# Kernel optimization log

Hardware: AMD Instinct MI355X
Metric: run time of the kernel (lower is better)

## Reference

```python
import math
import jax, jax.numpy as jnp
import numpy as np

B, L, D = 2, 2048, 512
H, DK, RANK, NH = 8, 64, 32, 1
K_MAX = 64
BANDWIDTH = 8.0
N_BUCKETS = 16


def setup_inputs() -> dict:
    key = jax.random.key(0)
    ks = jax.random.split(key, 14)
    s = 0.02
    return {
        "query": jax.random.normal(ks[0], (B, L, D), jnp.float32),
        "key": jax.random.normal(ks[1], (B, L, D), jnp.float32),
        "value": jax.random.normal(ks[2], (B, L, D), jnp.float32),
        "Wq": jax.random.normal(ks[3], (D, H * DK), jnp.float32) * s,
        "bq": jnp.zeros((H * DK,), jnp.float32),
        "Wk": jax.random.normal(ks[4], (D, H * DK), jnp.float32) * s,
        "bk": jnp.zeros((H * DK,), jnp.float32),
        "Wv": jax.random.normal(ks[5], (D, H * DK), jnp.float32) * s,
        "bv": jnp.zeros((H * DK,), jnp.float32),
        "U": jax.random.normal(ks[6], (H, DK, RANK), jnp.float32) * s,
        "V": jax.random.normal(ks[7], (H, RANK, D), jnp.float32) * s,
        "rv": jax.random.normal(ks[8], (H, DK, NH), jnp.float32),  # LSH random vectors (buffer)
        "Wo": jax.random.normal(ks[9], (H * D, D), jnp.float32) * s,
        "bo": jnp.zeros((D,), jnp.float32),
    }


def _lsh_hash(x, r):
    # binary quantize then bucketed floor hash: [B,L,dk] @ [dk,nh] -> [B,L,nh]
    xb = (x > 0).astype(x.dtype)
    return jnp.floor((xb @ r) / BANDWIDTH) % N_BUCKETS


def reference(query, key, value, Wq, bq, Wk, bk, Wv, bv, U, V, rv, Wo, bo):
    Bq, Lq, Dm = query.shape
    nheads, dk = U.shape[0], U.shape[1]
    q = (query @ Wq + bq).reshape(Bq, Lq, nheads, dk).transpose(0, 2, 1, 3)  # [B,H,L,dk]
    k = (key @ Wk + bk).reshape(Bq, Lq, nheads, dk).transpose(0, 2, 1, 3)
    v = (value @ Wv + bv).reshape(Bq, Lq, nheads, dk).transpose(0, 2, 1, 3)
    scale = math.sqrt(dk)  # optimized_sqrt(d_key), d_key power of two

    head_outputs = []
    for h in range(nheads):
        qh, kh, vh = q[:, h], k[:, h], v[:, h]  # [B,L,dk]
        qhash = _lsh_hash(qh, rv[h])  # [B,L,nh]
        khash = _lsh_hash(kh, rv[h])
        # [B,L,L] candidate match matrix (all hashes equal)
        matches = (qhash[:, :, None, :] == khash[:, None, :, :]).all(-1)
        # first K_MAX matching key indices in ascending order (== torch nonzero order)
        order = jnp.argsort(jnp.logical_not(matches), axis=-1, stable=True)
        cand = order[:, :, :K_MAX]  # [B,L,k_max]
        valid = jnp.take_along_axis(matches, cand, axis=-1)  # [B,L,k_max]
        ckeys = jnp.take_along_axis(kh[:, None, :, :], cand[..., None], axis=2)  # [B,L,k_max,dk]
        cvals = jnp.take_along_axis(vh[:, None, :, :], cand[..., None], axis=2)
        sim = jnp.einsum('bld,blkd->blk', qh, ckeys) / scale
        sim = jnp.where(valid, sim, -jnp.inf)
        attn = jax.nn.softmax(sim, axis=-1)  # invalid slots get exactly 0 weight
        # attention-weighted sum then low-rank up-projection (linear, so commutes
        # with the weighted sum; avoids the [B,L,k_max,d_model] intermediate)
        ctx = jnp.einsum('blk,blkd->bld', attn, cvals)  # [B,L,dk]
        head_outputs.append((ctx @ U[h]) @ V[h])  # [B,L,d_model]

    concat = jnp.concatenate(head_outputs, axis=-1)  # [B,L,H*d_model]
    return concat @ Wo + bo
```

## Files before the change

kernel.cpp:

```cpp
#include <hip/hip_runtime.h>
#include <math.h>

#define Bb 2
#define Ll 2048
#define Dd 512
#define Hh 8
#define DKq 64
#define NBUCK 16
#define KMAX 64
#define MAX_ITEMS 2304

__device__ __forceinline__ void gl_lds16(const float* g, float* l) {
  __builtin_amdgcn_global_load_lds(
      (const __attribute__((address_space(1))) void*)g,
      (__attribute__((address_space(3))) void*)l, 16, 0, 0);
}

#define VM_WAIT(N)                                                \
  do {                                                            \
    asm volatile("s_waitcnt vmcnt(" #N ")" ::: "memory");         \
    __builtin_amdgcn_sched_barrier(0);                            \
  } while (0)

__global__ __launch_bounds__(64) void proj_kernel(
    const float* __restrict__ Xq, const float* __restrict__ Xk, const float* __restrict__ Xv,
    const float* __restrict__ Wq, const float* __restrict__ Wk, const float* __restrict__ Wv,
    const float* __restrict__ bq, const float* __restrict__ bk, const float* __restrict__ bv,
    float* __restrict__ qb, float* __restrict__ kb, float* __restrict__ vb)
{
  const float *X, *W, *bias; float* dst;
  if (blockIdx.z == 0)      { X=Xq; W=Wq; bias=bq; dst=qb; }
  else if (blockIdx.z == 1) { X=Xk; W=Wk; bias=bk; dst=kb; }
  else                      { X=Xv; W=Wv; bias=bv; dst=vb; }
  __shared__ float Bs[3][16 * 64];
  const int lane = threadIdx.x;
  const int m0 = blockIdx.y * 32;
  const int n0 = blockIdx.x * 64;
  const int tx = lane & 15, ty = lane >> 4;

  const float* bSrc[4];
  #pragma unroll
  for (int j = 0; j < 4; j++) {
    int krow = 4*j + (lane >> 4);
    bSrc[j] = W + (size_t)krow * 512 + n0 + ((lane & 15) << 2);
  }
  const float* Arow[8];
  #pragma unroll
  for (int i = 0; i < 8; i++) Arow[i] = X + (size_t)(m0 + ty*8 + i) * 512;

  #pragma unroll
  for (int j = 0; j < 4; j++) gl_lds16(bSrc[j],                  &Bs[0][j*256]);
  #pragma unroll
  for (int j = 0; j < 4; j++) gl_lds16(bSrc[j] + (size_t)16*512, &Bs[1][j*256]);

  float acc[8][4] = {};
  int rd = 0, wr = 2;
  for (int t = 0; t < 32; t++) {
    if (t < 30) {
      const int ks = (t + 2) * 16;
      #pragma unroll
      for (int j = 0; j < 4; j++) gl_lds16(bSrc[j] + (size_t)ks*512, &Bs[wr][j*256]);
    }
    if (t == 0)       VM_WAIT(8);
    else if (t < 30)  VM_WAIT(40);
    else if (t == 30) VM_WAIT(36);
    else              VM_WAIT(32);

    const float* Bc = &Bs[rd][0];
    const int k0 = t * 16;
    float4 a[8], an[8];
    #pragma unroll
    for (int i = 0; i < 8; i++) a[i] = *(const float4*)&Arow[i][k0];
    #pragma unroll
    for (int kk4 = 0; kk4 < 4; kk4++) {
      if (kk4 < 3) {
        #pragma unroll
        for (int i = 0; i < 8; i++)
          an[i] = *(const float4*)&Arow[i][k0 + (kk4 + 1) * 4];
      }
      #pragma unroll
      for (int s = 0; s < 4; s++) {
        const int kk = kk4*4 + s;
        float4 b0 = *(const float4*)&Bc[kk*64 + tx*4];
        #pragma unroll
        for (int i = 0; i < 8; i++) {
          const float as = (s==0) ? a[i].x : (s==1) ? a[i].y
                         : (s==2) ? a[i].z : a[i].w;
          acc[i][0] += as * b0.x;  acc[i][1] += as * b0.y;
          acc[i][2] += as * b0.z;  acc[i][3] += as * b0.w;
        }
      }
      if (kk4 < 3) {
        #pragma unroll
        for (int i = 0; i < 8; i++) a[i] = an[i];
      }
    }
    rd = (rd == 2) ? 0 : rd + 1;
    wr = (wr == 2) ? 0 : wr + 1;
  }

  const int head = n0 >> 6;
  const int d0 = tx * 4;
  #pragma unroll
  for (int i = 0; i < 8; i++) {
    int m = m0 + ty*8 + i;
    int b = m >> 11, l = m & 2047;
    float* drow = &dst[(((size_t)b*Hh + head)*Ll + l)*DKq];
    #pragma unroll
    for (int j = 0; j < 4; j++) drow[d0 + j] = acc[i][j] + bias[n0 + tx*4 + j];
  }
}

__global__ __launch_bounds__(256) void hash_kernel(
    const float* __restrict__ qb, const float* __restrict__ kb,
    const float* __restrict__ rv, int* __restrict__ qhash, int* __restrict__ khash)
{
  int gwave = (blockIdx.x * blockDim.x + threadIdx.x) >> 6;
  int lane = threadIdx.x & 63;
  const int NR = Bb * Hh * Ll;
  if (gwave >= 2 * NR) return;
  int isK = gwave >= NR;
  int row = isK ? gwave - NR : gwave;
  int h = (row >> 11) & 7;
  const float* src = isK ? kb : qb;
  float x = src[(size_t)row * DKq + lane];
  float r = rv[h * DKq + lane];
  float v = (x > 0.0f) ? r : 0.0f;
  #pragma unroll
  for (int off = 32; off; off >>= 1) v += __shfl_xor(v, off);
  if (lane == 0) {
    float fb = floorf(v * 0.125f);
    int ib = (int)fb;
    int bucket = ib & 15;
    (isK ? khash : qhash)[row] = bucket;
  }
}

__global__ __launch_bounds__(256) void bucket_kernel(
    const int* __restrict__ qhash, const int* __restrict__ khash,
    int* __restrict__ qlist, int* __restrict__ kcand,
    int4* __restrict__ items, int* __restrict__ nitems)
{
  const int bh = blockIdx.x;
  const int tid = threadIdx.x;
  __shared__ int cnt[NBUCK], cur[NBUCK], off[NBUCK + 1], kc[NBUCK];
  if (tid < NBUCK) cnt[tid] = 0;
  __syncthreads();
  const int* qh = &qhash[bh * Ll];
  for (int l = tid; l < Ll; l += 256) atomicAdd(&cnt[qh[l]], 1);
  __syncthreads();
  if (tid == 0) {
    int s = 0;
    for (int i = 0; i < NBUCK; i++) { off[i] = s; cur[i] = s; s += cnt[i]; }
    off[NBUCK] = s;
  }
  __syncthreads();
  for (int l = tid; l < Ll; l += 256) {
    int p = atomicAdd(&cur[qh[l]], 1);
    qlist[bh * Ll + p] = l;
  }
  const int lane = tid & 63, w = tid >> 6;
  const int* kh = &khash[bh * Ll];
  for (int bi = 0; bi < 4; bi++) {
    int bucket = w * 4 + bi;
    int* cl = &kcand[((size_t)bh * NBUCK + bucket) * KMAX];
    int total = 0;
    for (int c0 = 0; c0 < Ll && total < KMAX; c0 += 64) {
      int hv = kh[c0 + lane];
      unsigned long long mm = __ballot(hv == bucket);
      int pre = __popcll(mm & ((1ULL << lane) - 1ULL));
      if (hv == bucket && total + pre < KMAX) cl[total + pre] = c0 + lane;
      total += __popcll(mm);
    }
    if (lane == 0) kc[bucket] = total < KMAX ? total : KMAX;
  }
  __syncthreads();
  if (tid < NBUCK) {
    const int bucket = tid;
    int nq = off[bucket + 1] - off[bucket];
    int cb = kc[bucket];
    int n = (cb > 0) ? ((nq + 15) >> 4) : 0;
    if (n > 0) {
      int base = atomicAdd(nitems, n);
      for (int i = 0; i < n; i++) {
        int q0 = 16 * i;
        int qn = nq - q0; if (qn > 16) qn = 16;
        items[base + i] = make_int4(bh * NBUCK + bucket, off[bucket] + q0, qn, cb);
      }
    }
  }
}

__device__ __forceinline__ void lds_fence() {
  asm volatile("s_waitcnt lgkmcnt(0)" ::: "memory");
  __builtin_amdgcn_sched_barrier(0);
}

__global__ __launch_bounds__(256, 2) void attn_kernel(
    const float* __restrict__ qb, const float* __restrict__ kb, const float* __restrict__ vb,
    const int* __restrict__ qlist, const int* __restrict__ kcand,
    const int4* __restrict__ items, const int* __restrict__ nitems,
    float* __restrict__ ctx)
{
  __shared__ float qs_all[4][16 * 64];
  __shared__ float sa_all[4][128];
  const int wid = threadIdx.x >> 6, lane = threadIdx.x & 63;
  const int idx = blockIdx.x * 4 + wid;
  if (idx >= nitems[0]) return;
  const int4 it = items[idx];
  const int code = it.x, qstart = it.y, qn = it.z, cnt = it.w;
  const int bh = code >> 4;
  float* qs = qs_all[wid];
  float* sa = sa_all[wid];

  const float* qbh = qb + (size_t)bh * Ll * DKq;
  const float* kbh = kb + (size_t)bh * Ll * DKq;
  const float* vbh = vb + (size_t)bh * Ll * DKq;

  int qidx_v = (lane < qn)  ? qlist[bh * Ll + qstart + lane] : 0;
  int cidx_v = (lane < cnt) ? kcand[(size_t)code * KMAX + lane] : 0;

  float4 kr[16];
  {
    const float4* krow = (const float4*)kbh + (size_t)cidx_v * 16;
    #pragma unroll
    for (int i = 0; i < 16; i++) kr[i] = krow[i];
  }
  float vt[64];
  #pragma unroll
  for (int c = 0; c < 64; c++) {
    int rowc = __shfl(cidx_v, c);
    vt[c] = vbh[(size_t)rowc * DKq + lane];
  }
  #pragma unroll
  for (int i = 0; i < 4; i++) {
    int f = lane + 64 * i;
    int r = f >> 4, c4 = f & 15;
    int qrow = __shfl(qidx_v, r);
    float4 qv = *((const float4*)qbh + (size_t)qrow * 16 + c4);
    *(float4*)&qs[r * 64 + c4 * 4] = qv;
  }
  lds_fence();

  const int b = bh >> 3, h = bh & 7;
  const float4* qs4 = (const float4*)qs;
  const float4* sa4 = (const float4*)sa;

  for (int jj = 0; jj < qn; jj += 2) {
    const int j0  = jj;
    const int j1v = jj + 1;
    const int j1r = (j1v < qn) ? j1v : j0;
    float p00=0.f,p01=0.f,p02=0.f,p03=0.f;
    float p10=0.f,p11=0.f,p12=0.f,p13=0.f;
    #pragma unroll
    for (int i = 0; i < 16; i += 4) {
      float4 qA0 = qs4[j0*16 + i + 0];
      float4 qA1 = qs4[j0*16 + i + 1];
      float4 qA2 = qs4[j0*16 + i + 2];
      float4 qA3 = qs4[j0*16 + i + 3];
      float4 qB0 = qs4[j1r*16 + i + 0];
      float4 qB1 = qs4[j1r*16 + i + 1];
      float4 qB2 = qs4[j1r*16 + i + 2];
      float4 qB3 = qs4[j1r*16 + i + 3];
      p00 += qA0.x*kr[i+0].x + qA0.y*kr[i+0].y + qA0.z*kr[i+0].z + qA0.w*kr[i+0].w;
      p01 += qA1.x*kr[i+1].x + qA1.y*kr[i+1].y + qA1.z*kr[i+1].z + qA1.w*kr[i+1].w;
      p02 += qA2.x*kr[i+2].x + qA2.y*kr[i+2].y + qA2.z*kr[i+2].z + qA2.w*kr[i+2].w;
      p03 += qA3.x*kr[i+3].x + qA3.y*kr[i+3].y + qA3.z*kr[i+3].z + qA3.w*kr[i+3].w;
      p10 += qB0.x*kr[i+0].x + qB0.y*kr[i+0].y + qB0.z*kr[i+0].z + qB0.w*kr[i+0].w;
      p11 += qB1.x*kr[i+1].x + qB1.y*kr[i+1].y + qB1.z*kr[i+1].z + qB1.w*kr[i+1].w;
      p12 += qB2.x*kr[i+2].x + qB2.y*kr[i+2].y + qB2.z*kr[i+2].z + qB2.w*kr[i+2].w;
      p13 += qB3.x*kr[i+3].x + qB3.y*kr[i+3].y + qB3.z*kr[i+3].z + qB3.w*kr[i+3].w;
    }
    float sA = ((p00 + p01) + (p02 + p03)) * 0.125f;
    float sB = ((p10 + p11) + (p12 + p13)) * 0.125f;
    sA = (lane < cnt) ? sA : -INFINITY;
    sB = (lane < cnt) ? sB : -INFINITY;
    float mA = sA, mB = sB;
    #pragma unroll
    for (int off = 32; off; off >>= 1) {
      mA = fmaxf(mA, __shfl_xor(mA, off));
      mB = fmaxf(mB, __shfl_xor(mB, off));
    }
    float eA = __expf(sA - mA);
    float eB = __expf(sB - mB);
    float sumA = eA, sumB = eB;
    #pragma unroll
    for (int off = 32; off; off >>= 1) {
      sumA += __shfl_xor(sumA, off);
      sumB += __shfl_xor(sumB, off);
    }
    lds_fence();
    sa[lane]      = eA;
    sa[64 + lane] = eB;
    lds_fence();
    float c00=0.f,c01=0.f,c02=0.f,c03=0.f;
    float c10=0.f,c11=0.f,c12=0.f,c13=0.f;
    #pragma unroll
    for (int i = 0; i < 16; i++) {
      float4 aA = sa4[i];
      float4 aB = sa4[16 + i];
      c00 += aA.x * vt[4*i + 0];
      c01 += aA.y * vt[4*i + 1];
      c02 += aA.z * vt[4*i + 2];
      c03 += aA.w * vt[4*i + 3];
      c10 += aB.x * vt[4*i + 0];
      c11 += aB.y * vt[4*i + 1];
      c12 += aB.z * vt[4*i + 2];
      c13 += aB.w * vt[4*i + 3];
    }
    {
      float ctxd = ((c00 + c01) + (c02 + c03)) / sumA;
      int qrow = __shfl(qidx_v, j0);
      ctx[((size_t)(b * Ll + qrow)) * 512 + h * 64 + lane] = ctxd;
    }
    if (j1v < qn) {
      float ctxd = ((c10 + c11) + (c12 + c13)) / sumB;
      int qrow = __shfl(qidx_v, j1v);
      ctx[((size_t)(b * Ll + qrow)) * 512 + h * 64 + lane] = ctxd;
    }
  }
}

__global__ __launch_bounds__(256) void uv_kernel(
    const float* __restrict__ U, const float* __restrict__ V, float* __restrict__ T)
{
  int idx = blockIdx.x * 256 + threadIdx.x;
  int n = idx & 511, dk = (idx >> 9) & 63, h = idx >> 15;
  float acc = 0.f;
  #pragma unroll
  for (int r = 0; r < 32; r++)
    acc += U[((size_t)h * 64 + dk) * 32 + r] * V[((size_t)h * 32 + r) * 512 + n];
  T[idx] = acc;
}

__global__ __launch_bounds__(64) void m_kernel(
    const float* __restrict__ T, const float* __restrict__ Wo, float* __restrict__ Mf)
{
  __shared__ float As[2][32 * 16];
  __shared__ float Bs[2][16 * 64];
  const int lane = threadIdx.x;
  const int h  = blockIdx.z;
  const int m0 = blockIdx.y * 32;
  const int n0 = blockIdx.x * 64;
  const int tx = lane & 15, ty = lane >> 4;

  const float* Tb = T + (size_t)h * 64 * 512;
  const float* Wb = Wo + (size_t)h * 512 * 512;

  const float* aSrc[2];
  #pragma unroll
  for (int j = 0; j < 2; j++) {
    int row  = 16*j + (lane >> 2);
    int key  = (row >> 3) & 3;
    int sK4  = (lane & 3) ^ key;
    aSrc[j] = Tb + (size_t)(m0 + row) * 512 + (sK4 << 2);
  }
  const float* bSrc[4];
  #pragma unroll
  for (int j = 0; j < 4; j++) {
    int krow = 4*j + (lane >> 4);
    bSrc[j] = Wb + (size_t)krow * 512 + n0 + ((lane & 15) << 2);
  }

  #pragma unroll
  for (int j = 0; j < 2; j++) gl_lds16(aSrc[j], &As[0][j*256]);
  #pragma unroll
  for (int j = 0; j < 4; j++) gl_lds16(bSrc[j], &Bs[0][j*256]);

  float acc[8][4] = {};
  for (int t = 0; t < 32; t++) {
    const int cur = t & 1;
    if (t < 31) {
      const int ks = (t + 1) * 16;
      const int nb = cur ^ 1;
      #pragma unroll
      for (int j = 0; j < 2; j++) gl_lds16(aSrc[j] + ks,              &As[nb][j*256]);
      #pragma unroll
      for (int j = 0; j < 4; j++) gl_lds16(bSrc[j] + (size_t)ks*512,  &Bs[nb][j*256]);
      VM_WAIT(6);
    } else {
      VM_WAIT(0);
    }

    const float* Ac = &As[cur][0];
    const float* Bc = &Bs[cur][0];
    #pragma unroll
    for (int kk4 = 0; kk4 < 4; kk4++) {
      float4 a[8];
      #pragma unroll
      for (int i = 0; i < 8; i++)
        a[i] = *(const float4*)&Ac[(ty*8 + i)*16 + ((kk4 ^ ty) << 2)];
      #pragma unroll
      for (int s = 0; s < 4; s++) {
        const int kk = kk4*4 + s;
        float4 b0 = *(const float4*)&Bc[kk*64 + tx*4];
        #pragma unroll
        for (int i = 0; i < 8; i++) {
          const float as = (s==0) ? a[i].x : (s==1) ? a[i].y
                         : (s==2) ? a[i].z : a[i].w;
          acc[i][0] += as * b0.x;  acc[i][1] += as * b0.y;
          acc[i][2] += as * b0.z;  acc[i][3] += as * b0.w;
        }
      }
    }
  }

  #pragma unroll
  for (int i = 0; i < 8; i++) {
    int row = h*64 + m0 + ty*8 + i;
    #pragma unroll
    for (int j = 0; j < 4; j++)
      Mf[(size_t)row * 512 + n0 + tx*4 + j] = acc[i][j];
  }
}

__global__ __launch_bounds__(64) void out_gemm(
    const float* __restrict__ A, const float* __restrict__ Bm,
    const float* __restrict__ bias, float* __restrict__ C)
{
  __shared__ float As[2][32 * 16];
  __shared__ float Bs[2][16 * 64];
  const int lane = threadIdx.x;
  const int m0 = blockIdx.y * 32;
  const int n0 = blockIdx.x * 64;
  const int tx = lane & 15, ty = lane >> 4;

  const float* aSrc[2];
  #pragma unroll
  for (int j = 0; j < 2; j++) {
    int row  = 16*j + (lane >> 2);
    int key  = (row >> 3) & 3;
    int sK4  = (lane & 3) ^ key;
    aSrc[j] = A + (size_t)(m0 + row) * 512 + (sK4 << 2);
  }
  const float* bSrc[4];
  #pragma unroll
  for (int j = 0; j < 4; j++) {
    int krow = 4*j + (lane >> 4);
    bSrc[j] = Bm + (size_t)krow * 512 + n0 + ((lane & 15) << 2);
  }

  #pragma unroll
  for (int j = 0; j < 2; j++) gl_lds16(aSrc[j], &As[0][j*256]);
  #pragma unroll
  for (int j = 0; j < 4; j++) gl_lds16(bSrc[j], &Bs[0][j*256]);

  float acc[8][4] = {};
  for (int t = 0; t < 32; t++) {
    const int cur = t & 1;
    if (t < 31) {
      const int ks = (t + 1) * 16;
      const int nb = cur ^ 1;
      #pragma unroll
      for (int j = 0; j < 2; j++) gl_lds16(aSrc[j] + ks,              &As[nb][j*256]);
      #pragma unroll
      for (int j = 0; j < 4; j++) gl_lds16(bSrc[j] + (size_t)ks*512,  &Bs[nb][j*256]);
      VM_WAIT(6);
    } else {
      VM_WAIT(0);
    }

    const float* Ac = &As[cur][0];
    const float* Bc = &Bs[cur][0];
    #pragma unroll
    for (int kk4 = 0; kk4 < 4; kk4++) {
      float4 a[8];
      #pragma unroll
      for (int i = 0; i < 8; i++)
        a[i] = *(const float4*)&Ac[(ty*8 + i)*16 + ((kk4 ^ ty) << 2)];
      #pragma unroll
      for (int s = 0; s < 4; s++) {
        const int kk = kk4*4 + s;
        float4 b0 = *(const float4*)&Bc[kk*64 + tx*4];
        #pragma unroll
        for (int i = 0; i < 8; i++) {
          const float as = (s==0) ? a[i].x : (s==1) ? a[i].y
                         : (s==2) ? a[i].z : a[i].w;
          acc[i][0] += as * b0.x;  acc[i][1] += as * b0.y;
          acc[i][2] += as * b0.z;  acc[i][3] += as * b0.w;
        }
      }
    }
  }

  #pragma unroll
  for (int i = 0; i < 8; i++) {
    int m = m0 + ty*8 + i;
    #pragma unroll
    for (int j = 0; j < 4; j++) {
      int n = n0 + tx*4 + j;
      C[(size_t)m * 512 + n] = acc[i][j] + bias[n];
    }
  }
}

extern "C" void kernel_launch(void* const* d_in, const int* in_sizes, int n_in,
                              void* d_out, int out_size, void* d_ws, size_t ws_size,
                              hipStream_t stream)
{
  const float* query = (const float*)d_in[0];
  const float* key   = (const float*)d_in[1];
  const float* value = (const float*)d_in[2];
  const float* Wq = (const float*)d_in[3];
  const float* bq = (const float*)d_in[4];
  const float* Wk = (const float*)d_in[5];
  const float* bk = (const float*)d_in[6];
  const float* Wv = (const float*)d_in[7];
  const float* bv = (const float*)d_in[8];
  const float* U  = (const float*)d_in[9];
  const float* V  = (const float*)d_in[10];
  const float* rv = (const float*)d_in[11];
  const float* Wo = (const float*)d_in[12];
  const float* bo = (const float*)d_in[13];
  float* out = (float*)d_out;

  float* ws = (float*)d_ws;
  const size_t NQKV = (size_t)Bb * Hh * Ll * DKq;
  float* qb   = ws;
  float* kb   = qb + NQKV;
  float* vb   = kb + NQKV;
  float* ctx  = vb + NQKV;
  float* T    = ctx + NQKV;
  float* Mf   = T + (size_t)Hh * DKq * 512;
  int* qhash  = (int*)(Mf + 512 * 512);
  int* khash  = qhash + Bb * Hh * Ll;
  int* kcand  = khash + Bb * Hh * Ll;
  int* kcount = kcand + Bb * Hh * NBUCK * KMAX;
  int* qoff   = kcount + Bb * Hh * NBUCK;
  int* qlist  = qoff + Bb * Hh * (NBUCK + 1);
  int4* items = (int4*)(qlist + Bb * Hh * Ll);
  int* nitems = (int*)(items + MAX_ITEMS);

  proj_kernel<<<dim3(8, 128, 3), 64, 0, stream>>>(query, key, value,
                                                  Wq, Wk, Wv, bq, bk, bv,
                                                  qb, kb, vb);
  hash_kernel<<<(2 * Bb * Hh * Ll * 64) / 256, 256, 0, stream>>>(qb, kb, rv, qhash, khash);
  hipMemsetAsync(nitems, 0, sizeof(int), stream);
  bucket_kernel<<<Bb * Hh, 256, 0, stream>>>(qhash, khash, qlist, kcand, items, nitems);
  attn_kernel<<<MAX_ITEMS / 4, 256, 0, stream>>>(qb, kb, vb, qlist, kcand,
                                                 items, nitems, ctx);
  uv_kernel<<<(Hh * DKq * 512) / 256, 256, 0, stream>>>(U, V, T);
  m_kernel<<<dim3(8, 2, 8), 64, 0, stream>>>(T, Wo, Mf);
  out_gemm<<<dim3(8, 128), 64, 0, stream>>>(ctx, Mf, bo, out);
}
```

Baseline: 274.0 us.

## Stage projection A tiles through LDS with swizzle and double buffering

In the QKV projection GEMM, the A (input activation) operand was read as direct per-thread float4 global loads. It is now staged into LDS with async global_load_lds, using an XOR swizzle on the k-chunk to avoid bank conflicts. The B pipeline drops from triple to double buffering so A and B share the same prefetch. This targets latency and redundant uncoalesced A global loads, at the cost of shallower prefetch depth and a wait on every iteration.

```diff
diff --git a/kernel.cpp b/kernel.cpp
--- a/kernel.cpp
+++ b/kernel.cpp
@@ -32,52 +32,56 @@
   if (blockIdx.z == 0)      { X=Xq; W=Wq; bias=bq; dst=qb; }
   else if (blockIdx.z == 1) { X=Xk; W=Wk; bias=bk; dst=kb; }
   else                      { X=Xv; W=Wv; bias=bv; dst=vb; }
-  __shared__ float Bs[3][16 * 64];
+  __shared__ float As[2][32 * 16];
+  __shared__ float Bs[2][16 * 64];
   const int lane = threadIdx.x;
   const int m0 = blockIdx.y * 32;
   const int n0 = blockIdx.x * 64;
   const int tx = lane & 15, ty = lane >> 4;
 
+  const float* aSrc[2];
+  #pragma unroll
+  for (int j = 0; j < 2; j++) {
+    int row  = 16*j + (lane >> 2);
+    int key  = (row >> 3) & 3;
+    int sK4  = (lane & 3) ^ key;
+    aSrc[j] = X + (size_t)(m0 + row) * 512 + (sK4 << 2);
+  }
   const float* bSrc[4];
   #pragma unroll
   for (int j = 0; j < 4; j++) {
     int krow = 4*j + (lane >> 4);
     bSrc[j] = W + (size_t)krow * 512 + n0 + ((lane & 15) << 2);
   }
-  const float* Arow[8];
-  #pragma unroll
-  for (int i = 0; i < 8; i++) Arow[i] = X + (size_t)(m0 + ty*8 + i) * 512;
-
-  #pragma unroll
-  for (int j = 0; j < 4; j++) gl_lds16(bSrc[j],                  &Bs[0][j*256]);
-  #pragma unroll
-  for (int j = 0; j < 4; j++) gl_lds16(bSrc[j] + (size_t)16*512, &Bs[1][j*256]);
+
+  #pragma unroll
+  for (int j = 0; j < 2; j++) gl_lds16(aSrc[j], &As[0][j*256]);
+  #pragma unroll
+  for (int j = 0; j < 4; j++) gl_lds16(bSrc[j], &Bs[0][j*256]);
 
   float acc[8][4] = {};
-  int rd = 0, wr = 2;
   for (int t = 0; t < 32; t++) {
-    if (t < 30) {
-      const int ks = (t + 2) * 16;
-      #pragma unroll
-      for (int j = 0; j < 4; j++) gl_lds16(bSrc[j] + (size_t)ks*512, &Bs[wr][j*256]);
-    }
-    if (t == 0)       VM_WAIT(8);
-    else if (t < 30)  VM_WAIT(40);
-    else if (t == 30) VM_WAIT(36);
-    else              VM_WAIT(32);
-
-    const float* Bc = &Bs[rd][0];
-    const int k0 = t * 16;
-    float4 a[8], an[8];
-    #pragma unroll
-    for (int i = 0; i < 8; i++) a[i] = *(const float4*)&Arow[i][k0];
+    const int cur = t & 1;
+    if (t < 31) {
+      const int ks = (t + 1) * 16;
+      const int nb = cur ^ 1;
+      #pragma unroll
+      for (int j = 0; j < 2; j++) gl_lds16(aSrc[j] + ks,              &As[nb][j*256]);
+      #pragma unroll
+      for (int j = 0; j < 4; j++) gl_lds16(bSrc[j] + (size_t)ks*512,  &Bs[nb][j*256]);
+      VM_WAIT(6);
+    } else {
+      VM_WAIT(0);
+    }
+
+    const float* Ac = &As[cur][0];
+    const float* Bc = &Bs[cur][0];
     #pragma unroll
     for (int kk4 = 0; kk4 < 4; kk4++) {
-      if (kk4 < 3) {
-        #pragma unroll
-        for (int i = 0; i < 8; i++)
-          an[i] = *(const float4*)&Arow[i][k0 + (kk4 + 1) * 4];
-      }
+      float4 a[8];
+      #pragma unroll
+      for (int i = 0; i < 8; i++)
+        a[i] = *(const float4*)&Ac[(ty*8 + i)*16 + ((kk4 ^ ty) << 2)];
       #pragma unroll
       for (int s = 0; s < 4; s++) {
         const int kk = kk4*4 + s;
@@ -90,13 +94,7 @@
           acc[i][2] += as * b0.z;  acc[i][3] += as * b0.w;
         }
       }
-      if (kk4 < 3) {
-        #pragma unroll
-        for (int i = 0; i < 8; i++) a[i] = an[i];
-      }
-    }
-    rd = (rd == 2) ? 0 : rd + 1;
-    wr = (wr == 2) ? 0 : wr + 1;
+    }
   }
 
   const int head = n0 >> 6;
```

New measurement: 257.0 us. 1.07x faster.
